# Performance work log

Measured on AMD Instinct MI355X. Metric: run time of the kernel, lower is better.

## Reference

```python
import jax, jax.numpy as jnp
import numpy as np

E, T, H, I, K = 16, 2048, 1024, 512, 2  # experts, tokens, hidden, intermediate, top_k


def setup_inputs() -> dict:
    key = jax.random.key(0)
    k1, k2, k3, k4, k5 = jax.random.split(key, 5)
    hidden_states = jax.random.normal(k1, (T, H), dtype=jnp.float32)
    topk_weights = jax.random.uniform(k2, (T, K), dtype=jnp.float32)
    topk_indices = jax.random.randint(k3, (T, K), 0, E, dtype=jnp.int32)
    # learned expert params, viewed per expert as in _view_experts_weight()
    gate_up_proj = jax.random.normal(k4, (E, H, 2 * I), dtype=jnp.float32) * 0.02
    down_proj = jax.random.normal(k5, (E, I, H), dtype=jnp.float32) * 0.02
    return {
        "hidden_states": hidden_states,
        "topk_weights": topk_weights,
        "topk_indices": topk_indices,
        "gate_up_proj": gate_up_proj,
        "down_proj": down_proj,
    }


def reference(hidden_states, topk_weights, topk_indices, gate_up_proj, down_proj):
    """MoE experts: per-expert gate_up GEMM -> silu-gate -> down GEMM,
    combined with top-k routing weights (index_add over tokens in the original).

    Equivalent dense formulation: combine[e, t] = sum_k topk_weights[t, k] * [topk_indices[t, k] == e];
    out = sum_e expert_e(hidden_states) * combine[e][:, None]. Tokens not routed to e get
    weight 0, matching the original gather/scatter-add exactly (including duplicate
    expert ids within a token, which accumulate).
    """
    num_experts = gate_up_proj.shape[0]
    one_hot = jax.nn.one_hot(topk_indices, num_experts, dtype=topk_weights.dtype)  # [T, K, E]
    combine = jnp.einsum("tk,tke->et", topk_weights, one_hot)  # [E, T]

    def body(acc, xs):
        w_gu, w_d, w = xs  # [H, 2I], [I, H], [T]
        gate_up = hidden_states @ w_gu  # [T, 2I]
        gate, up = jnp.split(gate_up, 2, axis=-1)
        expert_out = (jax.nn.silu(gate) * up) @ w_d  # [T, H]
        return acc + expert_out * w[:, None], None

    init = jnp.zeros_like(hidden_states)
    out, _ = jax.lax.scan(body, init, (gate_up_proj, down_proj, combine))
    return out.astype(hidden_states.dtype)
```

## Files before the change

### kernel.cpp

```cpp
#include <hip/hip_runtime.h>

#define E_ 16
#define T_ 2048
#define H_ 1024
#define I_ 512
#define NPAIR 4096
#define BM 128
#define MAXTILE 48

typedef __bf16 bf16x8 __attribute__((ext_vector_type(8)));
typedef float  f32x4  __attribute__((ext_vector_type(4)));

static __device__ __forceinline__ unsigned short f2bf(float f) {
    __bf16 h = (__bf16)f;
    return __builtin_bit_cast(unsigned short, h);
}

static __device__ __forceinline__ uint4 pack8(const float* v) {
    union { unsigned short us[8]; uint4 u; } r;
    #pragma unroll
    for (int i = 0; i < 8; ++i) r.us[i] = f2bf(v[i]);
    return r.u;
}

static __device__ __forceinline__ void gl_lds16(const void* g, void* l) {
    __builtin_amdgcn_global_load_lds(
        (const __attribute__((address_space(1))) unsigned int*)g,
        (__attribute__((address_space(3))) unsigned int*)l,
        16, 0, 0);
}

__global__ __launch_bounds__(256) void route_kernel(
    const float* __restrict__ tw, const int* __restrict__ ti,
    int* __restrict__ offs, int* __restrict__ tile_e, int* __restrict__ tile_r,
    int* __restrict__ pair_ts, float* __restrict__ pair_w)
{
    __shared__ unsigned short hist[256][E_];
    __shared__ int ebase[E_];
    const int tid = threadIdx.x;

    int e_loc[16];
    unsigned short h[E_];
    for (int e = 0; e < E_; ++e) h[e] = 0;
    for (int i = 0; i < 16; ++i) {
        int p = tid * 16 + i;
        int e = ti[p];
        e_loc[i] = e;
        h[e]++;
    }
    for (int e = 0; e < E_; ++e) hist[tid][e] = h[e];
    __syncthreads();

    if (tid < E_) {
        int e = tid, run = 0;
        for (int t = 0; t < 256; ++t) {
            unsigned short c = hist[t][e];
            hist[t][e] = (unsigned short)run;
            run += c;
        }
        ebase[e] = run;
    }
    __syncthreads();
    if (tid == 0) {
        int run = 0, nt = 0;
        for (int e = 0; e < E_; ++e) {
            int c = ebase[e];
            offs[e] = run; ebase[e] = run;
            for (int r = 0; r < c; r += BM) { tile_e[nt] = e; tile_r[nt] = r; ++nt; }
            run += c;
        }
        offs[E_] = run;
        for (; nt < MAXTILE; ++nt) tile_e[nt] = -1;
    }
    __syncthreads();

    int cur[E_];
    for (int e = 0; e < E_; ++e) cur[e] = ebase[e] + hist[tid][e];
    for (int i = 0; i < 16; ++i) {
        int p = tid * 16 + i;
        int e = e_loc[i];
        int pos = cur[e]++;
        pair_ts[pos] = p;
        pair_w[pos]  = tw[p];
    }
}

__global__ __launch_bounds__(256) void gather_kernel(
    const float* __restrict__ X, const int* __restrict__ pair_ts,
    unsigned short* __restrict__ Ag)
{
    const int q = blockIdx.x;
    const int t = pair_ts[q] >> 1;
    const int c = threadIdx.x * 4;
    const float4 x = *(const float4*)&X[(size_t)t * H_ + c];
    ushort4 b; b.x = f2bf(x.x); b.y = f2bf(x.y); b.z = f2bf(x.z); b.w = f2bf(x.w);
    *(ushort4*)&Ag[(size_t)q * H_ + c] = b;
}

__global__ __launch_bounds__(256) void transform_kernel(
    const float* __restrict__ W1, const float* __restrict__ W2,
    unsigned short* __restrict__ W1t, unsigned short* __restrict__ W2t)
{
    __shared__ float tile[64][65];
    const int t   = threadIdx.x;
    const int bid = blockIdx.x;

    if (bid < 4096) {
        const int cb = bid & 15, ks = (bid >> 4) & 15, e = bid >> 8;
        const float* __restrict__ W1e = W1 + (size_t)e * (H_ * 2 * I_);
        #pragma unroll
        for (int i = 0; i < 4; ++i) {
            int fi = i * 256 + t;
            int row = fi >> 4, c4 = fi & 15;
            const float* s = (c4 < 8)
                ? (W1e + (size_t)(ks * 64 + row) * (2 * I_) + cb * 32 + c4 * 4)
                : (W1e + (size_t)(ks * 64 + row) * (2 * I_) + I_ + cb * 32 + (c4 - 8) * 4);
            *(float4*)&tile[row][c4 * 4] = *(const float4*)s;
        }
        __syncthreads();
        unsigned short* __restrict__ dst =
            W1t + ((size_t)(e * 16 + cb) * 16 + ks) * 4096;
        #pragma unroll
        for (int s2 = 0; s2 < 2; ++s2) {
            int gidx = t * 2 + s2;
            int bn = gidx >> 3, p = gidx & 7;
            int kl = (p ^ (bn & 7)) * 8;
            int c  = ((bn >> 4) & 1) * 32 + (bn >> 5) * 16 + (bn & 15);
            float v[8];
            #pragma unroll
            for (int j = 0; j < 8; ++j) v[j] = tile[kl + j][c];
            *(uint4*)&dst[(size_t)gidx * 8] = pack8(v);
        }
    } else {
        const int b2 = bid - 4096;
        const int hb = b2 & 15, ks = (b2 >> 4) & 7, e = b2 >> 7;
        const float* __restrict__ W2e = W2 + (size_t)e * (I_ * H_);
        #pragma unroll
        for (int i = 0; i < 4; ++i) {
            int fi = i * 256 + t;
            int row = fi >> 4, c4 = fi & 15;
            *(float4*)&tile[row][c4 * 4] =
                *(const float4*)(W2e + (size_t)(ks * 64 + row) * H_ + hb * 64 + c4 * 4);
        }
        __syncthreads();
        unsigned short* __restrict__ dst =
            W2t + ((size_t)(e * 16 + hb) * 8 + ks) * 4096;
        #pragma unroll
        for (int s2 = 0; s2 < 2; ++s2) {
            int gidx = t * 2 + s2;
            int bn = gidx >> 3, p = gidx & 7;
            int kl = (p ^ (bn & 7)) * 8;
            float v[8];
            #pragma unroll
            for (int j = 0; j < 8; ++j) v[j] = tile[kl + j][bn];
            *(uint4*)&dst[(size_t)gidx * 8] = pack8(v);
        }
    }
}

#define MFMA_TILE(AS, BS)                                                              \
    _Pragma("unroll")                                                                  \
    for (int kkj = 0; kkj < 2; ++kkj) {                                                \
        const int j0 = kkj * 4;                                                        \
        bf16x8 af[4], bfr[2];                                                          \
        _Pragma("unroll")                                                              \
        for (int m = 0; m < 4; ++m)                                                    \
            af[m] = *(const bf16x8*)&AS[wm * 64 + m * 16 + lrow][((j0 + lk) ^ (lrow & 7)) * 8]; \
        _Pragma("unroll")                                                              \
        for (int n = 0; n < 2; ++n)                                                    \
            bfr[n] = *(const bf16x8*)&BS[wn * 32 + n * 16 + lrow][((j0 + lk) ^ (lrow & 7)) * 8]; \
        _Pragma("unroll")                                                              \
        for (int m = 0; m < 4; ++m)                                                    \
            _Pragma("unroll")                                                          \
            for (int n = 0; n < 2; ++n)                                                \
                acc[m][n] = __builtin_amdgcn_mfma_f32_16x16x32_bf16(af[m], bfr[n], acc[m][n], 0, 0, 0); \
    }

#define STAGE_A(BUF, KB)                                                               \
    _Pragma("unroll")                                                                  \
    for (int i = 0; i < 4; ++i) gl_lds16(asrc[i] + (KB), &As[BUF][w * 32 + i * 8][0]);

#define STAGE_B(BUF, KS)                                                               \
    _Pragma("unroll")                                                                  \
    for (int i = 0; i < 2; ++i)                                                        \
        gl_lds16(bsrcB + (size_t)(KS) * 4096 + i * 512,                                \
                 &Bs[BUF][0][0] + w * 1024 + i * 512);

#define K_PIPE(NT)                                                                     \
    STAGE_A(0, 0)                                                                      \
    STAGE_B(0, 0)                                                                      \
    __syncthreads();                                                                   \
    int cur = 0;                                                                       \
    _Pragma("unroll")                                                                  \
    for (int kt = 0; kt < (NT); ++kt) {                                                \
        int nxt = cur ^ 1;                                                             \
        if (kt + 1 < (NT)) { STAGE_A(nxt, (kt + 1) * 64) STAGE_B(nxt, kt + 1) }        \
        __builtin_amdgcn_s_setprio(1);                                                 \
        MFMA_TILE(As[cur], Bs[cur])                                                    \
        __builtin_amdgcn_s_setprio(0);                                                 \
        __syncthreads();                                                               \
        cur = nxt;                                                                     \
    }

__global__ __launch_bounds__(256, 3) void gemm1_kernel(
    const unsigned short* __restrict__ Ag, const unsigned short* __restrict__ W1t,
    const int* __restrict__ offs, const int* __restrict__ tile_e,
    const int* __restrict__ tile_r, unsigned short* __restrict__ act)
{
    const int e = tile_e[blockIdx.y];
    if (e < 0) return;
    const int rbeg = offs[e], rend = offs[e + 1];
    const int ne   = rend - rbeg;
    const int row0 = tile_r[blockIdx.y];
    const int cb   = blockIdx.x;
    const int c0   = cb * 32;

    __shared__ unsigned short As[2][128][64];
    __shared__ unsigned short Bs[2][64][64];

    const int tid  = threadIdx.x;
    const int lane = tid & 63;
    const int w    = tid >> 6;
    const int wm   = w >> 1, wn = w & 1;
    const int lrow = lane & 15;
    const int lk   = lane >> 4;

    const int r8 = lane >> 3, gr = lane & 7;
    const unsigned short* asrc[4];
    #pragma unroll
    for (int i = 0; i < 4; ++i) {
        int q = rbeg + row0 + w * 32 + i * 8 + r8;
        if (q > rend - 1) q = rend - 1;
        asrc[i] = Ag + (size_t)q * H_ + (gr ^ r8) * 8;
    }

    const unsigned short* bsrcB =
        W1t + ((size_t)(e * 16 + cb) * 16) * 4096 + w * 1024 + lane * 8;

    f32x4 acc[4][2];
    #pragma unroll
    for (int m = 0; m < 4; ++m)
        #pragma unroll
        for (int n = 0; n < 2; ++n)
            acc[m][n] = f32x4{0.f, 0.f, 0.f, 0.f};

    K_PIPE(16)

    for (int m = 0; m < 4; ++m) {
        #pragma unroll
        for (int reg = 0; reg < 4; ++reg) {
            int rloc = wm * 64 + m * 16 + lk * 4 + reg;
            if (row0 + rloc < ne) {
                int q = rbeg + row0 + rloc;
                float g = acc[m][0][reg], u = acc[m][1][reg];
                float a = g / (1.f + __expf(-g)) * u;
                act[(size_t)q * I_ + c0 + wn * 16 + lrow] = f2bf(a);
            }
        }
    }
}

__global__ __launch_bounds__(256, 3) void gemm2_kernel(
    const unsigned short* __restrict__ Agact, const unsigned short* __restrict__ W2t,
    const int* __restrict__ offs, const int* __restrict__ tile_e,
    const int* __restrict__ tile_r, const int* __restrict__ pair_ts,
    const float* __restrict__ pair_w, float* __restrict__ out)
{
    const int e = tile_e[blockIdx.y];
    if (e < 0) return;
    const int rbeg = offs[e], rend = offs[e + 1];
    const int ne   = rend - rbeg;
    const int row0 = tile_r[blockIdx.y];
    const int hb   = blockIdx.x;
    const int c0   = hb * 64;

    __shared__ unsigned short As[2][128][64];
    __shared__ unsigned short Bs[2][64][64];

    const int tid  = threadIdx.x;
    const int lane = tid & 63;
    const int w    = tid >> 6;
    const int wm   = w >> 1, wn = w & 1;
    const int lrow = lane & 15;
    const int lk   = lane >> 4;

    const int r8 = lane >> 3, gr = lane & 7;
    const unsigned short* asrc[4];
    #pragma unroll
    for (int i = 0; i < 4; ++i) {
        int q = rbeg + row0 + w * 32 + i * 8 + r8;
        if (q > rend - 1) q = rend - 1;
        asrc[i] = Agact + (size_t)q * I_ + (gr ^ r8) * 8;
    }

    const unsigned short* bsrcB =
        W2t + ((size_t)(e * 16 + hb) * 8) * 4096 + w * 1024 + lane * 8;

    f32x4 acc[4][2];
    #pragma unroll
    for (int m = 0; m < 4; ++m)
        #pragma unroll
        for (int n = 0; n < 2; ++n)
            acc[m][n] = f32x4{0.f, 0.f, 0.f, 0.f};

    K_PIPE(8)

    for (int m = 0; m < 4; ++m) {
        #pragma unroll
        for (int reg = 0; reg < 4; ++reg) {
            int rloc = wm * 64 + m * 16 + lk * 4 + reg;
            if (row0 + rloc < ne) {
                int q   = rbeg + row0 + rloc;
                int t   = pair_ts[q] >> 1;
                float wt = pair_w[q];
                #pragma unroll
                for (int n = 0; n < 2; ++n) {
                    int cg = c0 + wn * 32 + n * 16 + lrow;
                    atomicAdd(&out[(size_t)t * H_ + cg], wt * acc[m][n][reg]);
                }
            }
        }
    }
}

extern "C" void kernel_launch(void* const* d_in, const int* in_sizes, int n_in,
                              void* d_out, int out_size, void* d_ws, size_t ws_size,
                              hipStream_t stream)
{
    const float* X  = (const float*)d_in[0];
    const float* tw = (const float*)d_in[1];
    const int*   ti = (const int*)d_in[2];
    const float* W1 = (const float*)d_in[3];
    const float* W2 = (const float*)d_in[4];
    float* out = (float*)d_out;

    char* ws = (char*)d_ws;
    int*   offs    = (int*)(ws);
    int*   tile_e  = (int*)(ws + 128);
    int*   tile_r  = (int*)(ws + 320);
    int*   pair_ts = (int*)(ws + 1024);
    float* pair_w  = (float*)(ws + 1024 + NPAIR * 4);
    unsigned short* Ag  = (unsigned short*)(ws + (size_t)(1u << 16));
    unsigned short* act = (unsigned short*)(ws + (size_t)(1u << 16) + 8388608);
    unsigned short* W1t = (unsigned short*)(ws + (size_t)(1u << 16) + 12582912);
    unsigned short* W2t = (unsigned short*)(ws + (size_t)(1u << 16) + 46137344);

    hipMemsetAsync(d_out, 0, (size_t)out_size * sizeof(float), stream);

    route_kernel<<<1, 256, 0, stream>>>(tw, ti, offs, tile_e, tile_r, pair_ts, pair_w);

    gather_kernel<<<NPAIR, 256, 0, stream>>>(X, pair_ts, Ag);

    transform_kernel<<<6144, 256, 0, stream>>>(W1, W2, W1t, W2t);

    gemm1_kernel<<<dim3(16, MAXTILE), 256, 0, stream>>>(Ag, W1t, offs, tile_e, tile_r, act);

    gemm2_kernel<<<dim3(16, MAXTILE), 256, 0, stream>>>(act, W2t, offs, tile_e, tile_r, pair_ts, pair_w, out);
}
```

Baseline: 93.48 us.

## Replace atomic scatter with per-pair buffer and combine kernel; batch weight transform

Instead of atomically adding weighted expert outputs into the output, gemm2 now writes each routed pair's weighted result to a dense fp32 buffer. A new combine kernel then sums each token's two pair rows using an inverse index built in the routing kernel. This removes the memset and atomic contention at the cost of an extra 16MB write and read. The weight transform kernel also now processes four K-slices per block with double-buffered LDS and register prefetch, and it is launched first.

```diff
diff --git a/kernel.cpp b/kernel.cpp
--- a/kernel.cpp
+++ b/kernel.cpp
@@ -30,10 +30,14 @@
         16, 0, 0);
 }
 
+#define RAW_BARRIER_LGKM                                                \
+    asm volatile("s_waitcnt lgkmcnt(0)" ::: "memory");                  \
+    asm volatile("s_barrier" ::: "memory");
+
 __global__ __launch_bounds__(256) void route_kernel(
     const float* __restrict__ tw, const int* __restrict__ ti,
     int* __restrict__ offs, int* __restrict__ tile_e, int* __restrict__ tile_r,
-    int* __restrict__ pair_ts, float* __restrict__ pair_w)
+    int* __restrict__ pair_ts, float* __restrict__ pair_w, int* __restrict__ inv)
 {
     __shared__ unsigned short hist[256][E_];
     __shared__ int ebase[E_];
@@ -82,6 +86,7 @@
         int pos = cur[e]++;
         pair_ts[pos] = p;
         pair_w[pos]  = tw[p];
+        inv[p]       = pos;
     }
 }
 
@@ -97,63 +102,92 @@
     *(ushort4*)&Ag[(size_t)q * H_ + c] = b;
 }
 
-__global__ __launch_bounds__(256) void transform_kernel(
+__global__ __launch_bounds__(256, 4) void transform_kernel(
     const float* __restrict__ W1, const float* __restrict__ W2,
     unsigned short* __restrict__ W1t, unsigned short* __restrict__ W2t)
 {
-    __shared__ float tile[64][65];
-    const int t   = threadIdx.x;
+    __shared__ float tile[2][64][65];
+    const int t  = threadIdx.x;
+    const int c4 = t & 15, r0 = t >> 4;
     const int bid = blockIdx.x;
-
-    if (bid < 4096) {
-        const int cb = bid & 15, ks = (bid >> 4) & 15, e = bid >> 8;
-        const float* __restrict__ W1e = W1 + (size_t)e * (H_ * 2 * I_);
-        #pragma unroll
-        for (int i = 0; i < 4; ++i) {
-            int fi = i * 256 + t;
-            int row = fi >> 4, c4 = fi & 15;
-            const float* s = (c4 < 8)
-                ? (W1e + (size_t)(ks * 64 + row) * (2 * I_) + cb * 32 + c4 * 4)
-                : (W1e + (size_t)(ks * 64 + row) * (2 * I_) + I_ + cb * 32 + (c4 - 8) * 4);
-            *(float4*)&tile[row][c4 * 4] = *(const float4*)s;
-        }
-        __syncthreads();
-        unsigned short* __restrict__ dst =
-            W1t + ((size_t)(e * 16 + cb) * 16 + ks) * 4096;
-        #pragma unroll
-        for (int s2 = 0; s2 < 2; ++s2) {
-            int gidx = t * 2 + s2;
-            int bn = gidx >> 3, p = gidx & 7;
-            int kl = (p ^ (bn & 7)) * 8;
-            int c  = ((bn >> 4) & 1) * 32 + (bn >> 5) * 16 + (bn & 15);
-            float v[8];
+    float4 r[4];
+
+    if (bid < 1024) {
+        const int cb = bid & 15, ksg = (bid >> 4) & 3, e = bid >> 6;
+        const float* __restrict__ src = W1 + (size_t)e * (H_ * 2 * I_)
+            + ((c4 < 8) ? (cb * 32 + c4 * 4) : (I_ + cb * 32 + (c4 - 8) * 4));
+        unsigned short* __restrict__ dstb =
+            W1t + ((size_t)(e * 16 + cb) * 16 + ksg * 4) * 4096;
+        const int ks0 = ksg * 4;
+
+        #pragma unroll
+        for (int i = 0; i < 4; ++i)
+            r[i] = *(const float4*)(src + (size_t)(ks0 * 64 + r0 + i * 16) * (2 * I_));
+        #pragma unroll
+        for (int i = 0; i < 4; ++i) *(float4*)&tile[0][r0 + i * 16][c4 * 4] = r[i];
+        RAW_BARRIER_LGKM
+        #pragma unroll
+        for (int s = 0; s < 4; ++s) {
+            if (s + 1 < 4) {
+                #pragma unroll
+                for (int i = 0; i < 4; ++i)
+                    r[i] = *(const float4*)(src + (size_t)((ks0 + s + 1) * 64 + r0 + i * 16) * (2 * I_));
+            }
+            unsigned short* __restrict__ dst = dstb + s * 4096;
             #pragma unroll
-            for (int j = 0; j < 8; ++j) v[j] = tile[kl + j][c];
-            *(uint4*)&dst[(size_t)gidx * 8] = pack8(v);
+            for (int s2 = 0; s2 < 2; ++s2) {
+                int gidx = t * 2 + s2, bn = gidx >> 3, p = gidx & 7;
+                int kl = (p ^ (bn & 7)) * 8;
+                int c  = ((bn >> 4) & 1) * 32 + (bn >> 5) * 16 + (bn & 15);
+                float v[8];
+                #pragma unroll
+                for (int j = 0; j < 8; ++j) v[j] = tile[s & 1][kl + j][c];
+                *(uint4*)&dst[(size_t)gidx * 8] = pack8(v);
+            }
+            if (s + 1 < 4) {
+                #pragma unroll
+                for (int i = 0; i < 4; ++i)
+                    *(float4*)&tile[(s + 1) & 1][r0 + i * 16][c4 * 4] = r[i];
+                RAW_BARRIER_LGKM
+            }
         }
     } else {
-        const int b2 = bid - 4096;
-        const int hb = b2 & 15, ks = (b2 >> 4) & 7, e = b2 >> 7;
-        const float* __restrict__ W2e = W2 + (size_t)e * (I_ * H_);
-        #pragma unroll
-        for (int i = 0; i < 4; ++i) {
-            int fi = i * 256 + t;
-            int row = fi >> 4, c4 = fi & 15;
-            *(float4*)&tile[row][c4 * 4] =
-                *(const float4*)(W2e + (size_t)(ks * 64 + row) * H_ + hb * 64 + c4 * 4);
-        }
-        __syncthreads();
-        unsigned short* __restrict__ dst =
-            W2t + ((size_t)(e * 16 + hb) * 8 + ks) * 4096;
-        #pragma unroll
-        for (int s2 = 0; s2 < 2; ++s2) {
-            int gidx = t * 2 + s2;
-            int bn = gidx >> 3, p = gidx & 7;
-            int kl = (p ^ (bn & 7)) * 8;
-            float v[8];
+        const int b2 = bid - 1024;
+        const int hb = b2 & 15, ksg = (b2 >> 4) & 1, e = b2 >> 5;
+        const float* __restrict__ src = W2 + (size_t)e * (I_ * H_) + hb * 64 + c4 * 4;
+        unsigned short* __restrict__ dstb =
+            W2t + ((size_t)(e * 16 + hb) * 8 + ksg * 4) * 4096;
+        const int ks0 = ksg * 4;
+
+        #pragma unroll
+        for (int i = 0; i < 4; ++i)
+            r[i] = *(const float4*)(src + (size_t)(ks0 * 64 + r0 + i * 16) * H_);
+        #pragma unroll
+        for (int i = 0; i < 4; ++i) *(float4*)&tile[0][r0 + i * 16][c4 * 4] = r[i];
+        RAW_BARRIER_LGKM
+        #pragma unroll
+        for (int s = 0; s < 4; ++s) {
+            if (s + 1 < 4) {
+                #pragma unroll
+                for (int i = 0; i < 4; ++i)
+                    r[i] = *(const float4*)(src + (size_t)((ks0 + s + 1) * 64 + r0 + i * 16) * H_);
+            }
+            unsigned short* __restrict__ dst = dstb + s * 4096;
             #pragma unroll
-            for (int j = 0; j < 8; ++j) v[j] = tile[kl + j][bn];
-            *(uint4*)&dst[(size_t)gidx * 8] = pack8(v);
+            for (int s2 = 0; s2 < 2; ++s2) {
+                int gidx = t * 2 + s2, bn = gidx >> 3, p = gidx & 7;
+                int kl = (p ^ (bn & 7)) * 8;
+                float v[8];
+                #pragma unroll
+                for (int j = 0; j < 8; ++j) v[j] = tile[s & 1][kl + j][bn];
+                *(uint4*)&dst[(size_t)gidx * 8] = pack8(v);
+            }
+            if (s + 1 < 4) {
+                #pragma unroll
+                for (int i = 0; i < 4; ++i)
+                    *(float4*)&tile[(s + 1) & 1][r0 + i * 16][c4 * 4] = r[i];
+                RAW_BARRIER_LGKM
+            }
         }
     }
 }
@@ -263,8 +297,8 @@
 __global__ __launch_bounds__(256, 3) void gemm2_kernel(
     const unsigned short* __restrict__ Agact, const unsigned short* __restrict__ W2t,
     const int* __restrict__ offs, const int* __restrict__ tile_e,
-    const int* __restrict__ tile_r, const int* __restrict__ pair_ts,
-    const float* __restrict__ pair_w, float* __restrict__ out)
+    const int* __restrict__ tile_r, const float* __restrict__ pair_w,
+    float* __restrict__ C2)
 {
     const int e = tile_e[blockIdx.y];
     if (e < 0) return;
@@ -311,16 +345,29 @@
             int rloc = wm * 64 + m * 16 + lk * 4 + reg;
             if (row0 + rloc < ne) {
                 int q   = rbeg + row0 + rloc;
-                int t   = pair_ts[q] >> 1;
                 float wt = pair_w[q];
                 #pragma unroll
                 for (int n = 0; n < 2; ++n) {
                     int cg = c0 + wn * 32 + n * 16 + lrow;
-                    atomicAdd(&out[(size_t)t * H_ + cg], wt * acc[m][n][reg]);
+                    C2[(size_t)q * H_ + cg] = wt * acc[m][n][reg];
                 }
             }
         }
     }
+}
+
+__global__ __launch_bounds__(256) void combine_kernel(
+    const float* __restrict__ C2, const int* __restrict__ inv,
+    float* __restrict__ out)
+{
+    const int t = blockIdx.x;
+    const int c = threadIdx.x * 4;
+    const int q0 = inv[2 * t], q1 = inv[2 * t + 1];
+    const float4 a = *(const float4*)&C2[(size_t)q0 * H_ + c];
+    const float4 b = *(const float4*)&C2[(size_t)q1 * H_ + c];
+    float4 o;
+    o.x = a.x + b.x; o.y = a.y + b.y; o.z = a.z + b.z; o.w = a.w + b.w;
+    *(float4*)&out[(size_t)t * H_ + c] = o;
 }
 
 extern "C" void kernel_launch(void* const* d_in, const int* in_sizes, int n_in,
@@ -340,20 +387,22 @@
     int*   tile_r  = (int*)(ws + 320);
     int*   pair_ts = (int*)(ws + 1024);
     float* pair_w  = (float*)(ws + 1024 + NPAIR * 4);
+    int*   inv     = (int*)(ws + 1024 + NPAIR * 8);
     unsigned short* Ag  = (unsigned short*)(ws + (size_t)(1u << 16));
     unsigned short* act = (unsigned short*)(ws + (size_t)(1u << 16) + 8388608);
     unsigned short* W1t = (unsigned short*)(ws + (size_t)(1u << 16) + 12582912);
     unsigned short* W2t = (unsigned short*)(ws + (size_t)(1u << 16) + 46137344);
-
-    hipMemsetAsync(d_out, 0, (size_t)out_size * sizeof(float), stream);
-
-    route_kernel<<<1, 256, 0, stream>>>(tw, ti, offs, tile_e, tile_r, pair_ts, pair_w);
+    float*          C2  = (float*)(ws + (size_t)(1u << 16) + 62914560);
+
+    transform_kernel<<<1536, 256, 0, stream>>>(W1, W2, W1t, W2t);
+
+    route_kernel<<<1, 256, 0, stream>>>(tw, ti, offs, tile_e, tile_r, pair_ts, pair_w, inv);
 
     gather_kernel<<<NPAIR, 256, 0, stream>>>(X, pair_ts, Ag);
 
-    transform_kernel<<<6144, 256, 0, stream>>>(W1, W2, W1t, W2t);
-
     gemm1_kernel<<<dim3(16, MAXTILE), 256, 0, stream>>>(Ag, W1t, offs, tile_e, tile_r, act);
 
-    gemm2_kernel<<<dim3(16, MAXTILE), 256, 0, stream>>>(act, W2t, offs, tile_e, tile_r, pair_ts, pair_w, out);
-}
+    gemm2_kernel<<<dim3(16, MAXTILE), 256, 0, stream>>>(act, W2t, offs, tile_e, tile_r, pair_w, C2);
+
+    combine_kernel<<<T_, 256, 0, stream>>>(C2, inv, out);
+}
```

Result: faster. 85.87 us (-8.1%).
